# Kernel tuning notes

Hardware: AMD Instinct MI355X
Metric: run time of the kernel (lower is better)

## Reference

```python
import jax, jax.numpy as jnp
import numpy as np

EPS = 1e-8

def setup_inputs() -> dict:
    key = jax.random.key(0)
    ks = jax.random.split(key, 10)
    N, IN, Z, C, H = 8192, 512, 128, 64, 50
    x = jax.random.normal(ks[0], (N, IN), dtype=jnp.float32)
    c = jax.random.randint(ks[1], (N, 1), 0, C, dtype=jnp.int64)
    z = jax.random.normal(ks[2], (N, Z), dtype=jnp.float32)
    # f_x MLP params (Linear(IN,50) -> ReLU -> Linear(50,Z))
    W1 = jax.random.normal(ks[3], (IN, H), dtype=jnp.float32) / np.sqrt(IN)
    b1 = jax.random.normal(ks[4], (H,), dtype=jnp.float32) * 0.01
    W2 = jax.random.normal(ks[5], (H, Z), dtype=jnp.float32) / np.sqrt(H)
    b2 = jax.random.normal(ks[6], (Z,), dtype=jnp.float32) * 0.01
    # f_z Linear(Z,Z)
    Wz = jax.random.normal(ks[7], (Z, Z), dtype=jnp.float32) / np.sqrt(Z)
    bz = jax.random.normal(ks[8], (Z,), dtype=jnp.float32) * 0.01
    # per-category bilinear weights w_s [C,Z,Z] (torch.randn init)
    Ws = jax.random.normal(ks[9], (C, Z, Z), dtype=jnp.float32)
    return {"x": x, "c": c, "z": z, "W1": W1, "b1": b1, "W2": W2, "b2": b2, "Wz": Wz, "bz": bz, "Ws": Ws}

def reference(x, c, z, W1, b1, W2, b2, Wz, bz, Ws):
    cf = c.reshape(-1)                                    # [N]
    fx = jax.nn.relu(x @ W1 + b1) @ W2 + b2               # [N,Z]
    fz = z @ Wz + bz                                      # [N,Z]
    # per-sample bilinear: u[n] = fx[n] @ Ws[c[n]]
    u = jnp.einsum('nd,nde->ne', fx, Ws[cf])              # [N,Z]
    T = jax.nn.softplus(jnp.einsum('ne,ne->n', u, fz))    # [N]
    # neg_T[i] = mean over j with c[j]==c[i] of softplus(fx[i] @ Ws[c[i]] @ fz[j])
    S = jax.nn.softplus(u @ fz.T)                         # [N,N]
    mask = (cf[:, None] == cf[None, :]).astype(S.dtype)   # [N,N]
    neg_T = (S * mask).sum(axis=1) / mask.sum(axis=1)     # [N]
    return jnp.log(T + EPS) - jnp.log(neg_T + EPS)
```

## Files before the change

### kernel.cpp

```cpp
#include <hip/hip_runtime.h>
#include <math.h>

#define N_   8192
#define IN_  512
#define ZD   128
#define CC   64
#define HD   50
#define EPSF 1e-8f

typedef float vf4 __attribute__((ext_vector_type(4)));
typedef __attribute__((ext_vector_type(8))) short bfrag;

#define MFMA16(a, b, c) __builtin_amdgcn_mfma_f32_16x16x32_bf16((a), (b), (c), 0, 0, 0)

__device__ __forceinline__ float softplus_f(float t) {
    return fmaxf(t, 0.f) + log1pf(expf(-fabsf(t)));
}
__device__ __forceinline__ unsigned short bf16_rn(float x) {
    unsigned int u = __float_as_uint(x);
    return (unsigned short)((u + 0x7fff + ((u >> 16) & 1)) >> 16);
}
__device__ __forceinline__ float bf16_f(unsigned short h) {
    return __uint_as_float(((unsigned int)h) << 16);
}
__device__ __forceinline__ void split8(const float* v, bfrag& hi, bfrag& lo) {
    #pragma unroll
    for (int e = 0; e < 8; ++e) {
        unsigned short h = bf16_rn(v[e]);
        ((short*)&hi)[e] = (short)h;
        ((short*)&lo)[e] = (short)bf16_rn(v[e] - bf16_f(h));
    }
}

__global__ __launch_bounds__(256) void k_pre(const int* __restrict__ c,
                                             const float* __restrict__ W1,
                                             const float* __restrict__ z,
                                             const float* __restrict__ Wz,
                                             const float* __restrict__ bz,
                                             const float* __restrict__ W2,
                                             const float* __restrict__ Ws,
                                             uint4* __restrict__ W1p,
                                             uint4* __restrict__ W2p,
                                             float* __restrict__ fz,
                                             unsigned short* __restrict__ fz_hi,
                                             unsigned short* __restrict__ Wst_hi,
                                             unsigned short* __restrict__ Wst_lo,
                                             int* __restrict__ counts,
                                             int* __restrict__ offsets,
                                             int* __restrict__ grouped) {
    __shared__ float smem[64 * 129];
    int tid = threadIdx.x;
    int b   = blockIdx.x;
    if (b < CC) {
        __shared__ int hist[CC];
        __shared__ int cursor;
        __shared__ int off_s;
        if (tid < CC) hist[tid] = 0;
        if (tid == 0) cursor = 0;
        __syncthreads();
        for (int i = tid; i < N_; i += 256) atomicAdd(&hist[c[i]], 1);
        __syncthreads();
        if (tid == 0) {
            int off = 0;
            for (int q = 0; q < b; ++q) off += hist[q];
            off_s = off;
            counts[b]  = hist[b];
            offsets[b] = off;
        }
        __syncthreads();
        int off = off_s;
        for (int i = tid; i < N_; i += 256) {
            if (c[i] == b) {
                int p = atomicAdd(&cursor, 1);
                grouped[off + p] = i;
            }
        }
    } else if (b < 80) {
        int unit = (b - 64) * 256 + tid;
        int lane = unit & 63, f = (unit >> 6) & 15, kc = unit >> 10;
        int nt = f >> 2, ks = f & 3;
        int n = nt * 16 + (lane & 15);
        int kbase = kc * 128 + ks * 32 + (lane >> 4) * 8;
        unsigned short hi8[8], lo8[8];
        #pragma unroll
        for (int j = 0; j < 8; ++j) {
            int k = kbase + j;
            float v = (n < HD) ? W1[k * HD + n] : 0.f;
            unsigned short h = bf16_rn(v);
            hi8[j] = h;
            lo8[j] = bf16_rn(v - bf16_f(h));
        }
        W1p[kc * 2048 + f * 64 + lane]        = *(uint4*)hi8;
        W1p[kc * 2048 + 1024 + f * 64 + lane] = *(uint4*)lo8;
    } else if (b < 84) {
        int unit = (b - 80) * 256 + tid;
        int lane = unit & 63, f = unit >> 6;
        int nt = f >> 1, ks = f & 1;
        int n = nt * 16 + (lane & 15);
        int kbase = ks * 32 + (lane >> 4) * 8;
        unsigned short hi8[8], lo8[8];
        #pragma unroll
        for (int j = 0; j < 8; ++j) {
            int k = kbase + j;
            float v = (k < HD) ? W2[k * ZD + n] : 0.f;
            unsigned short h = bf16_rn(v);
            hi8[j] = h;
            lo8[j] = bf16_rn(v - bf16_f(h));
        }
        W2p[f * 64 + lane]        = *(uint4*)hi8;
        W2p[1024 + f * 64 + lane] = *(uint4*)lo8;
    } else if (b < 340) {
        float* sz = smem;
        int row0 = (b - 84) * 32;
        vf4* s4 = (vf4*)sz;
        const vf4* z4 = (const vf4*)(z + (size_t)row0 * ZD);
        #pragma unroll
        for (int f = 0; f < 4; ++f) s4[tid + f * 256] = z4[tid + f * 256];
        __syncthreads();
        int cp = tid & 31, rg = tid >> 5;
        const vf4* Wz4 = (const vf4*)Wz;
        vf4 bb = ((const vf4*)bz)[cp];
        vf4 acc[4];
        #pragma unroll
        for (int r = 0; r < 4; ++r) acc[r] = bb;
        #pragma unroll 1
        for (int d4 = 0; d4 < 32; ++d4) {
            vf4 w0 = Wz4[(4 * d4 + 0) * 32 + cp];
            vf4 w1 = Wz4[(4 * d4 + 1) * 32 + cp];
            vf4 w2 = Wz4[(4 * d4 + 2) * 32 + cp];
            vf4 w3 = Wz4[(4 * d4 + 3) * 32 + cp];
            #pragma unroll
            for (int r = 0; r < 4; ++r) {
                vf4 a = s4[(rg * 4 + r) * 32 + d4];
                acc[r] += a[0] * w0;
                acc[r] += a[1] * w1;
                acc[r] += a[2] * w2;
                acc[r] += a[3] * w3;
            }
        }
        vf4* fz4 = (vf4*)fz;
        #pragma unroll
        for (int r = 0; r < 4; ++r) {
            int n = row0 + rg * 4 + r;
            fz4[(size_t)n * 32 + cp] = acc[r];
            ushort4 h;
            h.x = bf16_rn(acc[r][0]); h.y = bf16_rn(acc[r][1]);
            h.z = bf16_rn(acc[r][2]); h.w = bf16_rn(acc[r][3]);
            *(ushort4*)(fz_hi + (size_t)n * ZD + cp * 4) = h;
        }
    } else {
        int cat = b - 340;
        const float* Wc = Ws + (size_t)cat * ZD * ZD;
        unsigned short* Whi = Wst_hi + (size_t)cat * ZD * ZD;
        unsigned short* Wlo = Wst_lo + (size_t)cat * ZD * ZD;
        #pragma unroll 1
        for (int half = 0; half < 2; ++half) {
            __syncthreads();
            const vf4* src = (const vf4*)(Wc + (size_t)half * 64 * ZD);
            #pragma unroll
            for (int f = 0; f < 8; ++f) {
                int idx = tid + f * 256;
                int row = idx >> 5, q = idx & 31;
                vf4 v = src[idx];
                #pragma unroll
                for (int e = 0; e < 4; ++e) smem[row * 129 + q * 4 + e] = v[e];
            }
            __syncthreads();
            #pragma unroll 1
            for (int f = 0; f < 32; ++f) {
                int idx = tid + f * 256;
                int e = idx >> 6, dd = idx & 63;
                float v = smem[dd * 129 + e];
                unsigned short h = bf16_rn(v);
                Whi[(size_t)e * ZD + half * 64 + dd] = h;
                Wlo[(size_t)e * ZD + half * 64 + dd] = bf16_rn(v - bf16_f(h));
            }
        }
    }
}

__global__ __launch_bounds__(256) void k_hfx(const float* __restrict__ x,
                                             const uint4* __restrict__ W1p,
                                             const uint4* __restrict__ W2p,
                                             const float* __restrict__ b1,
                                             const float* __restrict__ b2,
                                             unsigned short* __restrict__ fx_hi,
                                             unsigned short* __restrict__ fx_lo) {
    __shared__ uint4 sW2[2048];
    __shared__ uint4 sW1[2048];
    __shared__ float sh[64 * 68];
    int tid = threadIdx.x;
    int lane = tid & 63, w = tid >> 6, m = lane & 15, quad = lane >> 4;
    int i0 = blockIdx.x * 64;

    #pragma unroll
    for (int f = 0; f < 8; ++f) sW2[tid + f * 256] = W2p[tid + f * 256];

    int row = i0 + w * 16 + m;
    const float4* xr = (const float4*)(x + (size_t)row * IN_);

    vf4 acc[4];
    #pragma unroll
    for (int nt = 0; nt < 4; ++nt) acc[nt] = (vf4){0.f, 0.f, 0.f, 0.f};

    #pragma unroll 1
    for (int kc = 0; kc < 4; ++kc) {
        __syncthreads();
        #pragma unroll
        for (int f = 0; f < 8; ++f)
            sW1[tid + f * 256] = W1p[kc * 2048 + tid + f * 256];
        __syncthreads();
        #pragma unroll 1
        for (int ks = 0; ks < 4; ++ks) {
            float4 xa = xr[kc * 32 + ks * 8 + quad * 2];
            float4 xb = xr[kc * 32 + ks * 8 + quad * 2 + 1];
            float xv[8] = {xa.x, xa.y, xa.z, xa.w, xb.x, xb.y, xb.z, xb.w};
            bfrag ah, al;
            split8(xv, ah, al);
            #pragma unroll
            for (int nt = 0; nt < 4; ++nt) {
                bfrag bh = *(const bfrag*)&sW1[(nt * 4 + ks) * 64 + lane];
                bfrag bl = *(const bfrag*)&sW1[1024 + (nt * 4 + ks) * 64 + lane];
                acc[nt] = MFMA16(ah, bh, acc[nt]);
                acc[nt] = MFMA16(ah, bl, acc[nt]);
                acc[nt] = MFMA16(al, bh, acc[nt]);
            }
        }
    }
    #pragma unroll
    for (int nt = 0; nt < 4; ++nt) {
        int col = nt * 16 + m;
        float bb = (col < HD) ? b1[col] : 0.f;
        #pragma unroll
        for (int r = 0; r < 4; ++r)
            sh[(w * 16 + quad * 4 + r) * 68 + col] = fmaxf(acc[nt][r] + bb, 0.f);
    }
    __syncthreads();

    bfrag ah2[2], al2[2];
    #pragma unroll
    for (int ks = 0; ks < 2; ++ks) {
        const float4* shp = (const float4*)&sh[(w * 16 + m) * 68 + ks * 32 + quad * 8];
        float4 ha = shp[0], hb = shp[1];
        float hv[8] = {ha.x, ha.y, ha.z, ha.w, hb.x, hb.y, hb.z, hb.w};
        split8(hv, ah2[ks], al2[ks]);
    }
    #pragma unroll 1
    for (int nt = 0; nt < 8; ++nt) {
        vf4 a2 = {0.f, 0.f, 0.f, 0.f};
        #pragma unroll
        for (int ks = 0; ks < 2; ++ks) {
            bfrag bh = *(const bfrag*)&sW2[(nt * 2 + ks) * 64 + lane];
            bfrag bl = *(const bfrag*)&sW2[1024 + (nt * 2 + ks) * 64 + lane];
            a2 = MFMA16(ah2[ks], bh, a2);
            a2 = MFMA16(ah2[ks], bl, a2);
            a2 = MFMA16(al2[ks], bh, a2);
        }
        int col = nt * 16 + m;
        float bb2 = b2[col];
        #pragma unroll
        for (int r = 0; r < 4; ++r) {
            size_t rg = (size_t)(i0 + w * 16 + quad * 4 + r);
            float v = a2[r] + bb2;
            unsigned short hh = bf16_rn(v);
            fx_hi[rg * ZD + col] = hh;
            fx_lo[rg * ZD + col] = bf16_rn(v - bf16_f(hh));
        }
    }
}

#define TI 4
__global__ __launch_bounds__(256) void k_fused(const unsigned short* __restrict__ fx_hi,
                                               const unsigned short* __restrict__ fx_lo,
                                               const unsigned short* __restrict__ Wst_hi,
                                               const unsigned short* __restrict__ Wst_lo,
                                               const float* __restrict__ fz,
                                               const unsigned short* __restrict__ fz_hi,
                                               const int* __restrict__ grouped,
                                               const int* __restrict__ offsets,
                                               const int* __restrict__ counts,
                                               float* __restrict__ out) {
    __shared__ uint4 sWhi[128 * 17];
    __shared__ uint4 sWlo[128 * 17];
    int tid = threadIdx.x;
    int cat = blockIdx.x >> 2;
    int t   = blockIdx.x & (TI - 1);
    int off = offsets[cat], cnt = counts[cat];
    int i0 = t * 64;
    if (i0 >= cnt) return;
    int mI = min(64, cnt - i0);

    int lane = tid & 63, wave = tid >> 6;
    int m = lane & 15, quad = lane >> 4;

    const uint4* gh = (const uint4*)(Wst_hi + (size_t)cat * ZD * ZD);
    const uint4* gl = (const uint4*)(Wst_lo + (size_t)cat * ZD * ZD);
    #pragma unroll
    for (int f = 0; f < 8; ++f) {
        int idx = tid + f * 256;
        int e = idx >> 4, q = idx & 15;
        sWhi[e * 17 + q] = gh[idx];
        sWlo[e * 17 + q] = gl[idx];
    }

    int irow = wave * 16 + m;
    int n_gA = grouped[off + i0 + min(irow, mI - 1)];
    const unsigned short* fhp = fx_hi + (size_t)n_gA * ZD + quad * 8;
    const unsigned short* flp = fx_lo + (size_t)n_gA * ZD + quad * 8;
    bfrag a_hi[4], a_lo[4];
    #pragma unroll
    for (int kb = 0; kb < 4; ++kb) {
        a_hi[kb] = *(const bfrag*)(fhp + kb * 32);
        a_lo[kb] = *(const bfrag*)(flp + kb * 32);
    }
    __syncthreads();

    vf4 uacc[8];
    #pragma unroll 1
    for (int et = 0; et < 8; ++et) {
        vf4 acc = {0.f, 0.f, 0.f, 0.f};
        #pragma unroll
        for (int kb = 0; kb < 4; ++kb) {
            bfrag bh = *(const bfrag*)&sWhi[(et * 16 + m) * 17 + kb * 4 + quad];
            bfrag bl = *(const bfrag*)&sWlo[(et * 16 + m) * 17 + kb * 4 + quad];
            acc = MFMA16(a_hi[kb], bh, acc);
            acc = MFMA16(a_hi[kb], bl, acc);
            acc = MFMA16(a_lo[kb], bh, acc);
        }
        uacc[et] = acc;
    }

    int nrow[4];
    float p[4] = {0.f, 0.f, 0.f, 0.f};
    #pragma unroll
    for (int r = 0; r < 4; ++r) {
        int ir = wave * 16 + quad * 4 + r;
        nrow[r] = (ir < mI) ? grouped[off + i0 + ir] : -1;
    }
    #pragma unroll 1
    for (int et = 0; et < 8; ++et) {
        #pragma unroll
        for (int r = 0; r < 4; ++r) {
            if (nrow[r] >= 0)
                p[r] += uacc[et][r] * fz[(size_t)nrow[r] * ZD + et * 16 + m];
        }
    }
    #pragma unroll
    for (int r = 0; r < 4; ++r) {
        float v = p[r];
        #pragma unroll
        for (int s = 8; s >= 1; s >>= 1) v += __shfl_xor(v, s, 64);
        p[r] = v;
    }
    float logT_r[4];
    #pragma unroll
    for (int r = 0; r < 4; ++r) logT_r[r] = logf(softplus_f(p[r]) + EPSF);

    __syncthreads();
    unsigned short* su = (unsigned short*)sWhi;
    #pragma unroll
    for (int et = 0; et < 8; ++et) {
        #pragma unroll
        for (int r = 0; r < 4; ++r) {
            int rowq = wave * 16 + quad * 4 + r;
            su[rowq * 136 + et * 16 + m] = bf16_rn(uacc[et][r]);
        }
    }
    __syncthreads();

    bfrag na[4];
    #pragma unroll
    for (int kb = 0; kb < 4; ++kb)
        na[kb] = *(const bfrag*)&su[(wave * 16 + m) * 136 + kb * 32 + quad * 8];

    uint4* sB = (uint4*)sWlo;
    float negsum[4] = {0.f, 0.f, 0.f, 0.f};

    #pragma unroll 1
    for (int jb = 0; jb < cnt; jb += 64) {
        int mJ = min(64, cnt - jb);
        __syncthreads();
        #pragma unroll
        for (int f = 0; f < 4; ++f) {
            int idx = tid + f * 256;
            int jr = idx >> 4, q = idx & 15;
            uint4 v = {0u, 0u, 0u, 0u};
            if (jr < mJ) {
                int j_g = grouped[off + jb + jr];
                v = *(const uint4*)(fz_hi + (size_t)j_g * ZD + q * 8);
            }
            sB[jr * 17 + q] = v;
        }
        __syncthreads();
        #pragma unroll 1
        for (int jt = 0; jt < 4; ++jt) {
            vf4 acc = {0.f, 0.f, 0.f, 0.f};
            #pragma unroll
            for (int kb = 0; kb < 4; ++kb) {
                bfrag bb = *(const bfrag*)&sB[(jt * 16 + m) * 17 + kb * 4 + quad];
                acc = MFMA16(na[kb], bb, acc);
            }
            bool jok = (jt * 16 + m) < mJ;
            #pragma unroll
            for (int r = 0; r < 4; ++r)
                if (jok) negsum[r] += softplus_f(acc[r]);
        }
    }

    #pragma unroll
    for (int r = 0; r < 4; ++r) {
        float v = negsum[r];
        #pragma unroll
        for (int s = 8; s >= 1; s >>= 1) v += __shfl_xor(v, s, 64);
        negsum[r] = v;
    }
    if (m == 0) {
        #pragma unroll
        for (int r = 0; r < 4; ++r) {
            if (nrow[r] >= 0)
                out[nrow[r]] = logT_r[r] - logf(negsum[r] / (float)cnt + EPSF);
        }
    }
}

extern "C" void kernel_launch(void* const* d_in, const int* in_sizes, int n_in,
                              void* d_out, int out_size, void* d_ws, size_t ws_size,
                              hipStream_t stream) {
    const float* x  = (const float*)d_in[0];
    const int*   c  = (const int*)  d_in[1];
    const float* z  = (const float*)d_in[2];
    const float* W1 = (const float*)d_in[3];
    const float* b1 = (const float*)d_in[4];
    const float* W2 = (const float*)d_in[5];
    const float* b2 = (const float*)d_in[6];
    const float* Wz = (const float*)d_in[7];
    const float* bz = (const float*)d_in[8];
    const float* Ws = (const float*)d_in[9];
    float* out = (float*)d_out;

    uint4* W1p = (uint4*)d_ws;
    uint4* W2p = W1p + 8192;
    float* fz  = (float*)(W2p + 2048);
    unsigned short* fx_hi  = (unsigned short*)(fz + (size_t)N_ * ZD);
    unsigned short* fx_lo  = fx_hi + (size_t)N_ * ZD;
    unsigned short* fz_hi  = fx_lo + (size_t)N_ * ZD;
    unsigned short* Wst_hi = fz_hi + (size_t)N_ * ZD;
    unsigned short* Wst_lo = Wst_hi + (size_t)CC * ZD * ZD;
    int* counts  = (int*)(Wst_lo + (size_t)CC * ZD * ZD);
    int* offsets = counts + CC;
    int* grouped = offsets + CC;

    k_pre   <<<404, 256, 0, stream>>>(c, W1, z, Wz, bz, W2, Ws, W1p, W2p, fz,
                                      fz_hi, Wst_hi, Wst_lo, counts, offsets,
                                      grouped);
    k_hfx   <<<N_ / 64, 256, 0, stream>>>(x, W1p, W2p, b1, b2, fx_hi, fx_lo);
    k_fused <<<CC * TI, 256, 0, stream>>>(fx_hi, fx_lo, Wst_hi, Wst_lo, fz,
                                          fz_hi, grouped, offsets, counts, out);
}
```

Measured before the change: 147.4 us.

## Rebalance work splits across pre, hfx and fused kernels; use fast softplus

The change halves the rows per block in k_hfx and k_fused and splits the output columns across wave pairs, which doubles the grid size and adds shared-memory reductions. It also gives the MFMA chains independent accumulators, merges Ws conversion into two categories per block, and doubles the rows per fz block in k_pre. The hot softplus now uses the fast __expf/__logf intrinsics instead of log1pf/expf. The aim is more parallelism and shorter dependency chains, at the cost of extra barriers and slightly lower softplus accuracy.

```diff
diff --git a/kernel.cpp b/kernel.cpp
--- a/kernel.cpp
+++ b/kernel.cpp
@@ -13,7 +13,10 @@
 
 #define MFMA16(a, b, c) __builtin_amdgcn_mfma_f32_16x16x32_bf16((a), (b), (c), 0, 0, 0)
 
-__device__ __forceinline__ float softplus_f(float t) {
+__device__ __forceinline__ float softplus_hot(float t) {
+    return fmaxf(t, 0.f) + __logf(1.f + __expf(-fabsf(t)));
+}
+__device__ __forceinline__ float softplus_acc(float t) {
     return fmaxf(t, 0.f) + log1pf(expf(-fabsf(t)));
 }
 __device__ __forceinline__ unsigned short bf16_rn(float x) {
@@ -109,20 +112,20 @@
         }
         W2p[f * 64 + lane]        = *(uint4*)hi8;
         W2p[1024 + f * 64 + lane] = *(uint4*)lo8;
-    } else if (b < 340) {
+    } else if (b < 212) {
         float* sz = smem;
-        int row0 = (b - 84) * 32;
+        int row0 = (b - 84) * 64;
         vf4* s4 = (vf4*)sz;
         const vf4* z4 = (const vf4*)(z + (size_t)row0 * ZD);
         #pragma unroll
-        for (int f = 0; f < 4; ++f) s4[tid + f * 256] = z4[tid + f * 256];
-        __syncthreads();
-        int cp = tid & 31, rg = tid >> 5;
+        for (int f = 0; f < 8; ++f) s4[tid + f * 256] = z4[tid + f * 256];
+        __syncthreads();
+        int cp = tid & 31, rgp = tid >> 5;
         const vf4* Wz4 = (const vf4*)Wz;
         vf4 bb = ((const vf4*)bz)[cp];
-        vf4 acc[4];
-        #pragma unroll
-        for (int r = 0; r < 4; ++r) acc[r] = bb;
+        vf4 acc[8];
+        #pragma unroll
+        for (int r = 0; r < 8; ++r) acc[r] = bb;
         #pragma unroll 1
         for (int d4 = 0; d4 < 32; ++d4) {
             vf4 w0 = Wz4[(4 * d4 + 0) * 32 + cp];
@@ -130,8 +133,8 @@
             vf4 w2 = Wz4[(4 * d4 + 2) * 32 + cp];
             vf4 w3 = Wz4[(4 * d4 + 3) * 32 + cp];
             #pragma unroll
-            for (int r = 0; r < 4; ++r) {
-                vf4 a = s4[(rg * 4 + r) * 32 + d4];
+            for (int r = 0; r < 8; ++r) {
+                vf4 a = s4[(rgp * 8 + r) * 32 + d4];
                 acc[r] += a[0] * w0;
                 acc[r] += a[1] * w1;
                 acc[r] += a[2] * w2;
@@ -140,8 +143,8 @@
         }
         vf4* fz4 = (vf4*)fz;
         #pragma unroll
-        for (int r = 0; r < 4; ++r) {
-            int n = row0 + rg * 4 + r;
+        for (int r = 0; r < 8; ++r) {
+            int n = row0 + rgp * 8 + r;
             fz4[(size_t)n * 32 + cp] = acc[r];
             ushort4 h;
             h.x = bf16_rn(acc[r][0]); h.y = bf16_rn(acc[r][1]);
@@ -149,31 +152,34 @@
             *(ushort4*)(fz_hi + (size_t)n * ZD + cp * 4) = h;
         }
     } else {
-        int cat = b - 340;
-        const float* Wc = Ws + (size_t)cat * ZD * ZD;
-        unsigned short* Whi = Wst_hi + (size_t)cat * ZD * ZD;
-        unsigned short* Wlo = Wst_lo + (size_t)cat * ZD * ZD;
         #pragma unroll 1
-        for (int half = 0; half < 2; ++half) {
-            __syncthreads();
-            const vf4* src = (const vf4*)(Wc + (size_t)half * 64 * ZD);
-            #pragma unroll
-            for (int f = 0; f < 8; ++f) {
-                int idx = tid + f * 256;
-                int row = idx >> 5, q = idx & 31;
-                vf4 v = src[idx];
+        for (int ci = 0; ci < 2; ++ci) {
+            int cat = (b - 212) * 2 + ci;
+            const float* Wc = Ws + (size_t)cat * ZD * ZD;
+            unsigned short* Whi = Wst_hi + (size_t)cat * ZD * ZD;
+            unsigned short* Wlo = Wst_lo + (size_t)cat * ZD * ZD;
+            #pragma unroll 1
+            for (int half = 0; half < 2; ++half) {
+                __syncthreads();
+                const vf4* src = (const vf4*)(Wc + (size_t)half * 64 * ZD);
                 #pragma unroll
-                for (int e = 0; e < 4; ++e) smem[row * 129 + q * 4 + e] = v[e];
-            }
-            __syncthreads();
-            #pragma unroll 1
-            for (int f = 0; f < 32; ++f) {
-                int idx = tid + f * 256;
-                int e = idx >> 6, dd = idx & 63;
-                float v = smem[dd * 129 + e];
-                unsigned short h = bf16_rn(v);
-                Whi[(size_t)e * ZD + half * 64 + dd] = h;
-                Wlo[(size_t)e * ZD + half * 64 + dd] = bf16_rn(v - bf16_f(h));
+                for (int f = 0; f < 8; ++f) {
+                    int idx = tid + f * 256;
+                    int row = idx >> 5, q = idx & 31;
+                    vf4 v = src[idx];
+                    #pragma unroll
+                    for (int e = 0; e < 4; ++e) smem[row * 129 + q * 4 + e] = v[e];
+                }
+                __syncthreads();
+                #pragma unroll 1
+                for (int f = 0; f < 32; ++f) {
+                    int idx = tid + f * 256;
+                    int e = idx >> 6, dd = idx & 63;
+                    float v = smem[dd * 129 + e];
+                    unsigned short h = bf16_rn(v);
+                    Whi[(size_t)e * ZD + half * 64 + dd] = h;
+                    Wlo[(size_t)e * ZD + half * 64 + dd] = bf16_rn(v - bf16_f(h));
+                }
             }
         }
     }
@@ -188,20 +194,24 @@
                                              unsigned short* __restrict__ fx_lo) {
     __shared__ uint4 sW2[2048];
     __shared__ uint4 sW1[2048];
-    __shared__ float sh[64 * 68];
+    __shared__ float sh[32 * 68];
     int tid = threadIdx.x;
     int lane = tid & 63, w = tid >> 6, m = lane & 15, quad = lane >> 4;
-    int i0 = blockIdx.x * 64;
+    int rg = w & 1, ch = w >> 1;
+    int i0 = blockIdx.x * 32;
 
     #pragma unroll
     for (int f = 0; f < 8; ++f) sW2[tid + f * 256] = W2p[tid + f * 256];
 
-    int row = i0 + w * 16 + m;
+    int row = i0 + rg * 16 + m;
     const float4* xr = (const float4*)(x + (size_t)row * IN_);
 
-    vf4 acc[4];
-    #pragma unroll
-    for (int nt = 0; nt < 4; ++nt) acc[nt] = (vf4){0.f, 0.f, 0.f, 0.f};
+    vf4 accP[2], accQ[2];
+    #pragma unroll
+    for (int nt2 = 0; nt2 < 2; ++nt2) {
+        accP[nt2] = (vf4){0.f, 0.f, 0.f, 0.f};
+        accQ[nt2] = (vf4){0.f, 0.f, 0.f, 0.f};
+    }
 
     #pragma unroll 1
     for (int kc = 0; kc < 4; ++kc) {
@@ -218,58 +228,65 @@
             bfrag ah, al;
             split8(xv, ah, al);
             #pragma unroll
-            for (int nt = 0; nt < 4; ++nt) {
+            for (int nt2 = 0; nt2 < 2; ++nt2) {
+                int nt = ch * 2 + nt2;
                 bfrag bh = *(const bfrag*)&sW1[(nt * 4 + ks) * 64 + lane];
                 bfrag bl = *(const bfrag*)&sW1[1024 + (nt * 4 + ks) * 64 + lane];
-                acc[nt] = MFMA16(ah, bh, acc[nt]);
-                acc[nt] = MFMA16(ah, bl, acc[nt]);
-                acc[nt] = MFMA16(al, bh, acc[nt]);
+                accP[nt2] = MFMA16(ah, bh, accP[nt2]);
+                accQ[nt2] = MFMA16(ah, bl, accQ[nt2]);
+                accQ[nt2] = MFMA16(al, bh, accQ[nt2]);
             }
         }
     }
     #pragma unroll
-    for (int nt = 0; nt < 4; ++nt) {
+    for (int nt2 = 0; nt2 < 2; ++nt2) {
+        int nt = ch * 2 + nt2;
         int col = nt * 16 + m;
         float bb = (col < HD) ? b1[col] : 0.f;
+        vf4 acc = accP[nt2] + accQ[nt2];
         #pragma unroll
         for (int r = 0; r < 4; ++r)
-            sh[(w * 16 + quad * 4 + r) * 68 + col] = fmaxf(acc[nt][r] + bb, 0.f);
+            sh[(rg * 16 + quad * 4 + r) * 68 + col] = fmaxf(acc[r] + bb, 0.f);
     }
     __syncthreads();
 
     bfrag ah2[2], al2[2];
     #pragma unroll
     for (int ks = 0; ks < 2; ++ks) {
-        const float4* shp = (const float4*)&sh[(w * 16 + m) * 68 + ks * 32 + quad * 8];
+        const float4* shp = (const float4*)&sh[(rg * 16 + m) * 68 + ks * 32 + quad * 8];
         float4 ha = shp[0], hb = shp[1];
         float hv[8] = {ha.x, ha.y, ha.z, ha.w, hb.x, hb.y, hb.z, hb.w};
         split8(hv, ah2[ks], al2[ks]);
     }
-    #pragma unroll 1
-    for (int nt = 0; nt < 8; ++nt) {
-        vf4 a2 = {0.f, 0.f, 0.f, 0.f};
-        #pragma unroll
-        for (int ks = 0; ks < 2; ++ks) {
-            bfrag bh = *(const bfrag*)&sW2[(nt * 2 + ks) * 64 + lane];
-            bfrag bl = *(const bfrag*)&sW2[1024 + (nt * 2 + ks) * 64 + lane];
-            a2 = MFMA16(ah2[ks], bh, a2);
-            a2 = MFMA16(ah2[ks], bl, a2);
-            a2 = MFMA16(al2[ks], bh, a2);
-        }
+    #pragma unroll 2
+    for (int nt2 = 0; nt2 < 4; ++nt2) {
+        int nt = ch * 4 + nt2;
+        bfrag bh0 = *(const bfrag*)&sW2[(nt * 2 + 0) * 64 + lane];
+        bfrag bl0 = *(const bfrag*)&sW2[1024 + (nt * 2 + 0) * 64 + lane];
+        bfrag bh1 = *(const bfrag*)&sW2[(nt * 2 + 1) * 64 + lane];
+        bfrag bl1 = *(const bfrag*)&sW2[1024 + (nt * 2 + 1) * 64 + lane];
+        vf4 aA = {0.f, 0.f, 0.f, 0.f}, aB = {0.f, 0.f, 0.f, 0.f};
+        aA = MFMA16(ah2[0], bh0, aA);
+        aA = MFMA16(ah2[0], bl0, aA);
+        aA = MFMA16(al2[0], bh0, aA);
+        aB = MFMA16(ah2[1], bh1, aB);
+        aB = MFMA16(ah2[1], bl1, aB);
+        aB = MFMA16(al2[1], bh1, aB);
+        vf4 a2 = aA + aB;
         int col = nt * 16 + m;
         float bb2 = b2[col];
         #pragma unroll
         for (int r = 0; r < 4; ++r) {
-            size_t rg = (size_t)(i0 + w * 16 + quad * 4 + r);
+            size_t orow = (size_t)(i0 + rg * 16 + quad * 4 + r);
             float v = a2[r] + bb2;
             unsigned short hh = bf16_rn(v);
-            fx_hi[rg * ZD + col] = hh;
-            fx_lo[rg * ZD + col] = bf16_rn(v - bf16_f(hh));
-        }
-    }
-}
-
-#define TI 4
+            fx_hi[orow * ZD + col] = hh;
+            fx_lo[orow * ZD + col] = bf16_rn(v - bf16_f(hh));
+        }
+    }
+}
+
+#define TI 8
 __global__ __launch_bounds__(256) void k_fused(const unsigned short* __restrict__ fx_hi,
                                                const unsigned short* __restrict__ fx_lo,
                                                const unsigned short* __restrict__ Wst_hi,
@@ -282,16 +299,18 @@
                                                float* __restrict__ out) {
     __shared__ uint4 sWhi[128 * 17];
     __shared__ uint4 sWlo[128 * 17];
+    __shared__ float sRed[2][2][16];
     int tid = threadIdx.x;
-    int cat = blockIdx.x >> 2;
+    int cat = blockIdx.x >> 3;
     int t   = blockIdx.x & (TI - 1);
     int off = offsets[cat], cnt = counts[cat];
-    int i0 = t * 64;
+    int i0 = t * 32;
     if (i0 >= cnt) return;
-    int mI = min(64, cnt - i0);
+    int mI = min(32, cnt - i0);
 
     int lane = tid & 63, wave = tid >> 6;
     int m = lane & 15, quad = lane >> 4;
+    int rg = wave & 1, eh = wave >> 1;
 
     const uint4* gh = (const uint4*)(Wst_hi + (size_t)cat * ZD * ZD);
     const uint4* gl = (const uint4*)(Wst_lo + (size_t)cat * ZD * ZD);
@@ -303,7 +322,7 @@
         sWlo[e * 17 + q] = gl[idx];
     }
 
-    int irow = wave * 16 + m;
+    int irow = rg * 16 + m;
     int n_gA = grouped[off + i0 + min(irow, mI - 1)];
     const unsigned short* fhp = fx_hi + (size_t)n_gA * ZD + quad * 8;
     const unsigned short* flp = fx_lo + (size_t)n_gA * ZD + quad * 8;
@@ -315,35 +334,45 @@
     }
     __syncthreads();
 
-    vf4 uacc[8];
+    vf4 uacc[4];
     #pragma unroll 1
-    for (int et = 0; et < 8; ++et) {
-        vf4 acc = {0.f, 0.f, 0.f, 0.f};
+    for (int et2 = 0; et2 < 4; ++et2) {
+        int et = eh * 4 + et2;
+        vf4 aH = {0.f, 0.f, 0.f, 0.f};
+        vf4 aM = {0.f, 0.f, 0.f, 0.f};
+        vf4 aL = {0.f, 0.f, 0.f, 0.f};
         #pragma unroll
         for (int kb = 0; kb < 4; ++kb) {
             bfrag bh = *(const bfrag*)&sWhi[(et * 16 + m) * 17 + kb * 4 + quad];
             bfrag bl = *(const bfrag*)&sWlo[(et * 16 + m) * 17 + kb * 4 + quad];
-            acc = MFMA16(a_hi[kb], bh, acc);
-            acc = MFMA16(a_hi[kb], bl, acc);
-            acc = MFMA16(a_lo[kb], bh, acc);
-        }
-        uacc[et] = acc;
+            aH = MFMA16(a_hi[kb], bh, aH);
+            aM = MFMA16(a_hi[kb], bl, aM);
+            aL = MFMA16(a_lo[kb], bh, aL);
+        }
+        uacc[et2] = aH + aM + aL;
     }
 
     int nrow[4];
+    #pragma unroll
+    for (int r = 0; r < 4; ++r) {
+        int ir = rg * 16 + quad * 4 + r;
+        nrow[r] = (ir < mI) ? grouped[off + i0 + ir] : -1;
+    }
+    float fzv[4][4];
+    #pragma unroll
+    for (int et2 = 0; et2 < 4; ++et2) {
+        #pragma unroll
+        for (int r = 0; r < 4; ++r) {
+            fzv[et2][r] = 0.f;
+            if (nrow[r] >= 0)
+                fzv[et2][r] = fz[(size_t)nrow[r] * ZD + (eh * 4 + et2) * 16 + m];
+        }
+    }
     float p[4] = {0.f, 0.f, 0.f, 0.f};
     #pragma unroll
-    for (int r = 0; r < 4; ++r) {
-        int ir = wave * 16 + quad * 4 + r;
-        nrow[r] = (ir < mI) ? grouped[off + i0 + ir] : -1;
-    }
-    #pragma unroll 1
-    for (int et = 0; et < 8; ++et) {
-        #pragma unroll
-        for (int r = 0; r < 4; ++r) {
-            if (nrow[r] >= 0)
-                p[r] += uacc[et][r] * fz[(size_t)nrow[r] * ZD + et * 16 + m];
-        }
+    for (int et2 = 0; et2 < 4; ++et2) {
+        #pragma unroll
+        for (int r = 0; r < 4; ++r) p[r] += uacc[et2][r] * fzv[et2][r];
     }
     #pragma unroll
     for (int r = 0; r < 4; ++r) {
@@ -352,18 +381,26 @@
         for (int s = 8; s >= 1; s >>= 1) v += __shfl_xor(v, s, 64);
         p[r] = v;
     }
-    float logT_r[4];
-    #pragma unroll
-    for (int r = 0; r < 4; ++r) logT_r[r] = logf(softplus_f(p[r]) + EPSF);
-
+    if (m == 0) {
+        #pragma unroll
+        for (int r = 0; r < 4; ++r) sRed[rg][eh][quad * 4 + r] = p[r];
+    }
     __syncthreads();
+
     unsigned short* su = (unsigned short*)sWhi;
     #pragma unroll
-    for (int et = 0; et < 8; ++et) {
+    for (int et2 = 0; et2 < 4; ++et2) {
+        int col = (eh * 4 + et2) * 16 + m;
+        #pragma unroll
+        for (int r = 0; r < 4; ++r)
+            su[(rg * 16 + quad * 4 + r) * 136 + col] = bf16_rn(uacc[et2][r]);
+    }
+    float logT_r[4] = {0.f, 0.f, 0.f, 0.f};
+    if (eh == 0) {
         #pragma unroll
         for (int r = 0; r < 4; ++r) {
-            int rowq = wave * 16 + quad * 4 + r;
-            su[rowq * 136 + et * 16 + m] = bf16_rn(uacc[et][r]);
+            float pt = sRed[rg][0][quad * 4 + r] + sRed[rg][1][quad * 4 + r];
+            logT_r[r] = logf(softplus_acc(pt) + EPSF);
         }
     }
     __syncthreads();
@@ -371,7 +408,7 @@
     bfrag na[4];
     #pragma unroll
     for (int kb = 0; kb < 4; ++kb)
-        na[kb] = *(const bfrag*)&su[(wave * 16 + m) * 136 + kb * 32 + quad * 8];
+        na[kb] = *(const bfrag*)&su[(rg * 16 + m) * 136 + kb * 32 + quad * 8];
 
     uint4* sB = (uint4*)sWlo;
     float negsum[4] = {0.f, 0.f, 0.f, 0.f};
@@ -392,18 +429,23 @@
             sB[jr * 17 + q] = v;
         }
         __syncthreads();
-        #pragma unroll 1
-        for (int jt = 0; jt < 4; ++jt) {
-            vf4 acc = {0.f, 0.f, 0.f, 0.f};
-            #pragma unroll
-            for (int kb = 0; kb < 4; ++kb) {
-                bfrag bb = *(const bfrag*)&sB[(jt * 16 + m) * 17 + kb * 4 + quad];
-                acc = MFMA16(na[kb], bb, acc);
-            }
+        #pragma unroll
+        for (int jt2 = 0; jt2 < 2; ++jt2) {
+            int jt = eh * 2 + jt2;
+            bfrag b0 = *(const bfrag*)&sB[(jt * 16 + m) * 17 + 0 + quad];
+            bfrag b1 = *(const bfrag*)&sB[(jt * 16 + m) * 17 + 4 + quad];
+            bfrag b2 = *(const bfrag*)&sB[(jt * 16 + m) * 17 + 8 + quad];
+            bfrag b3 = *(const bfrag*)&sB[(jt * 16 + m) * 17 + 12 + quad];
+            vf4 aA = {0.f, 0.f, 0.f, 0.f}, aB = {0.f, 0.f, 0.f, 0.f};
+            aA = MFMA16(na[0], b0, aA);
+            aA = MFMA16(na[1], b1, aA);
+            aB = MFMA16(na[2], b2, aB);
+            aB = MFMA16(na[3], b3, aB);
+            vf4 acc = aA + aB;
             bool jok = (jt * 16 + m) < mJ;
             #pragma unroll
             for (int r = 0; r < 4; ++r)
-                if (jok) negsum[r] += softplus_f(acc[r]);
+                if (jok) negsum[r] += softplus_hot(acc[r]);
         }
     }
 
@@ -416,9 +458,16 @@
     }
     if (m == 0) {
         #pragma unroll
+        for (int r = 0; r < 4; ++r) sRed[rg][eh][quad * 4 + r] = negsum[r];
+    }
+    __syncthreads();
+    if (eh == 0 && m == 0) {
+        #pragma unroll
         for (int r = 0; r < 4; ++r) {
-            if (nrow[r] >= 0)
-                out[nrow[r]] = logT_r[r] - logf(negsum[r] / (float)cnt + EPSF);
+            if (nrow[r] >= 0) {
+                float tot = sRed[rg][0][quad * 4 + r] + sRed[rg][1][quad * 4 + r];
+                out[nrow[r]] = logT_r[r] - logf(tot / (float)cnt + EPSF);
+            }
         }
     }
 }
@@ -450,10 +499,10 @@
     int* offsets = counts + CC;
     int* grouped = offsets + CC;
 
-    k_pre   <<<404, 256, 0, stream>>>(c, W1, z, Wz, bz, W2, Ws, W1p, W2p, fz,
+    k_pre   <<<244, 256, 0, stream>>>(c, W1, z, Wz, bz, W2, Ws, W1p, W2p, fz,
                                       fz_hi, Wst_hi, Wst_lo, counts, offsets,
                                       grouped);
-    k_hfx   <<<N_ / 64, 256, 0, stream>>>(x, W1p, W2p, b1, b2, fx_hi, fx_lo);
+    k_hfx   <<<N_ / 32, 256, 0, stream>>>(x, W1p, W2p, b1, b2, fx_hi, fx_lo);
     k_fused <<<CC * TI, 256, 0, stream>>>(fx_hi, fx_lo, Wst_hi, Wst_lo, fz,
                                           fz_hi, grouped, offsets, counts, out);
 }
```

After: 131.7 us. -10.6%, faster.
